# Performance work log

Hardware: AMD Instinct MI355X
Metric: run time of the kernel (lower is better)

The kernel has to match this reference:

```python
import jax, jax.numpy as jnp
import numpy as np

B, E, F, H, P = 1024, 300, 128, 512, 256


def _gru_cell(x, h, Wih, Whh, bih, bhh):
    # PyTorch GRUCell: gates ordered (r, z, n)
    gi = x @ Wih.T + bih
    gh = h @ Whh.T + bhh
    i_r, i_z, i_n = jnp.split(gi, 3, axis=-1)
    h_r, h_z, h_n = jnp.split(gh, 3, axis=-1)
    r = jax.nn.sigmoid(i_r + h_r)
    z = jax.nn.sigmoid(i_z + h_z)
    n = jnp.tanh(i_n + r * h_n)
    return (1.0 - z) * n + z * h


def setup_inputs() -> dict:
    key = jax.random.key(0)
    ks = jax.random.split(key, 24)
    rn = lambda k, s: (jax.random.normal(k, s, dtype=jnp.float32) * 0.05)
    inp = {
        'step_input': jax.random.normal(ks[0], (B, E), dtype=jnp.float32),
        'target_feat': jax.random.normal(ks[1], (B, F), dtype=jnp.float32),
        'obj_feats': jax.random.normal(ks[2], (B, P, F), dtype=jnp.float32),
        'hidden_1': jax.random.normal(ks[3], (B, H), dtype=jnp.float32),
        'hidden_2': jax.random.normal(ks[4], (B, H), dtype=jnp.float32),
        # Linear weights, shape (out, in), bias=False
        'W_td1': rn(ks[5], (128, H)),
        'W_td2': rn(ks[6], (128, F)),
        'W_td3': rn(ks[7], (128, E)),
        'W_td': rn(ks[8], (128, 128)),
        'W_feat': rn(ks[9], (H, F)),
        'W_hidd': rn(ks[10], (H, H)),
        'W_att': rn(ks[11], (1, H)),
        'W_l1': rn(ks[12], (128, F)),
        'W_l2': rn(ks[13], (128, H)),
        'W_l': rn(ks[14], (128, 128)),
        # GRUCell params (bias=True by default in torch)
        'gru1_Wih': rn(ks[15], (3 * H, 128)),
        'gru1_Whh': rn(ks[16], (3 * H, H)),
        'gru1_bih': rn(ks[17], (3 * H,)),
        'gru1_bhh': rn(ks[18], (3 * H,)),
        'gru2_Wih': rn(ks[19], (3 * H, 128)),
        'gru2_Whh': rn(ks[20], (3 * H, H)),
        'gru2_bih': rn(ks[21], (3 * H,)),
        'gru2_bhh': rn(ks[22], (3 * H,)),
    }
    return inp


def reference(step_input, target_feat, obj_feats, hidden_1, hidden_2,
              W_td1, W_td2, W_td3, W_td,
              W_feat, W_hidd, W_att, W_l1, W_l2, W_l,
              gru1_Wih, gru1_Whh, gru1_bih, gru1_bhh,
              gru2_Wih, gru2_Whh, gru2_bih, gru2_bhh):
    # Top-down input fusion
    td = step_input @ W_td3.T + hidden_2 @ W_td1.T + target_feat @ W_td2.T
    td = jax.nn.relu(jnp.tanh(td) @ W_td.T)
    h1 = _gru_cell(td, hidden_1, gru1_Wih, gru1_Whh, gru1_bih, gru1_bhh)

    # Soft attention over proposals
    combined = jnp.tanh(
        jnp.einsum('bpf,hf->bph', obj_feats, W_feat)
        + (h1 @ W_hidd.T)[:, None, :]
    )  # (B, P, H)
    scores = jnp.einsum('bph,oh->bpo', combined, W_att)  # (B, P, 1)
    masks = jax.nn.softmax(scores, axis=1)  # (B, P, 1)
    attended = jnp.sum(obj_feats * masks, axis=1)  # (B, F)

    # Language input fusion
    lang = jnp.tanh(attended @ W_l1.T + h1 @ W_l2.T)
    lang = jax.nn.relu(lang @ W_l.T)
    h2 = _gru_cell(lang, hidden_2, gru2_Wih, gru2_Whh, gru2_bih, gru2_bhh)
    return (h1, h2, masks)
```

## Files before the change

kernel.cpp:

```cpp
#include <hip/hip_runtime.h>
#include <hip/hip_bf16.h>
#include <stdint.h>


typedef __attribute__((ext_vector_type(8))) short short8;
typedef __attribute__((ext_vector_type(4))) float f32x4;

#define DEV static __device__ __forceinline__

DEV float rcp_f(float x) { return __builtin_amdgcn_rcpf(x); }
DEV float fast_tanh(float x) {
  float ax = fabsf(x);
  float e = __expf(2.0f * ax);
  float t = 1.0f - 2.0f * rcp_f(e + 1.0f);
  return x < 0.0f ? -t : t;
}
DEV float fast_sigmoid(float x) { return rcp_f(1.0f + __expf(-x)); }
DEV unsigned short f2bf(float x) {
  unsigned u = __float_as_uint(x);
  u += 0x7fffu + ((u >> 16) & 1u);
  return (unsigned short)(u >> 16);
}
DEV float bf2f(unsigned short s) { return __uint_as_float(((unsigned)s) << 16); }

#define NJOBS 17
struct CvtJobs {
  const float* src[NJOBS];
  unsigned short* dst[NJOBS];
};
__global__ __launch_bounds__(256) void cvt_all(CvtJobs jobs) {
  const int cum[NJOBS + 1] = {0, 327680, 458752, 983040, 1507328, 1548288,
                              1613824, 1630208, 1646592, 1712128, 1974272,
                              1990656, 2056192, 2072576, 2269184, 3055616,
                              3252224, 4038656};
  const int Ks[NJOBS]  = {300, 128, 512, 512, 300, 512, 128, 128, 128, 512,
                          128, 512, 128, 128, 512, 128, 512};
  const int Kps[NJOBS] = {320, 128, 512, 512, 320, 512, 128, 128, 128, 512,
                          128, 512, 128, 128, 512, 128, 512};
  int g = blockIdx.x * 256 + (int)threadIdx.x;
  if (g >= 4038656) return;
  int j = 0;
  while (g >= cum[j + 1]) ++j;
  const int local = g - cum[j];
  const int Kp = Kps[j], K = Ks[j];
  const int r = local / Kp, c = local - r * Kp;
  jobs.dst[j][local] = (c < K) ? f2bf(jobs.src[j][(size_t)r * K + c])
                               : (unsigned short)0;
}

#define FACC 1
#define FRELU (1 << 2)
#define FTANH (2 << 2)
__global__ __launch_bounds__(256) void gemm_bf16(
    const unsigned short* __restrict__ A, const unsigned short* __restrict__ W,
    const float* __restrict__ bias, float* __restrict__ C,
    unsigned short* __restrict__ Cb, int M, int N, int K,
    int lda, int ldw, int flags)
{
  __shared__ unsigned short As[64][40];
  __shared__ unsigned short Ws[64][40];
  const int bm = blockIdx.x * 64, bn = blockIdx.y * 64;
  const int tid = (int)threadIdx.x;
  const int w = tid >> 6, l = tid & 63, l15 = l & 15, lg = l >> 4;
  const int wr = w >> 1, wc = w & 1;
  const int srow = tid >> 2, sq = tid & 3;

  f32x4 acc[2][2] = {};

  for (int k0 = 0; k0 < K; k0 += 32) {
    const uint4 va = *(const uint4*)(A + (size_t)(bm + srow) * lda + k0 + sq * 8);
    const uint4 vw = *(const uint4*)(W + (size_t)(bn + srow) * ldw + k0 + sq * 8);
    __syncthreads();
    *(uint4*)&As[srow][sq * 8] = va;
    *(uint4*)&Ws[srow][sq * 8] = vw;
    __syncthreads();

    short8 af[2], bf[2];
#pragma unroll
    for (int mi = 0; mi < 2; ++mi) {
      const int ar = wr * 32 + mi * 16 + l15;
      union { short8 s8; uint2 u[2]; } f;
      f.u[0] = *(const uint2*)&As[ar][lg * 4];
      f.u[1] = *(const uint2*)&As[ar][16 + lg * 4];
      af[mi] = f.s8;
    }
#pragma unroll
    for (int ni = 0; ni < 2; ++ni) {
      const int br = wc * 32 + ni * 16 + l15;
      union { short8 s8; uint2 u[2]; } f;
      f.u[0] = *(const uint2*)&Ws[br][lg * 4];
      f.u[1] = *(const uint2*)&Ws[br][16 + lg * 4];
      bf[ni] = f.s8;
    }
#pragma unroll
    for (int mi = 0; mi < 2; ++mi)
#pragma unroll
      for (int ni = 0; ni < 2; ++ni)
        acc[mi][ni] = __builtin_amdgcn_mfma_f32_16x16x32_bf16(
            af[mi], bf[ni], acc[mi][ni], 0, 0, 0);
  }

  const int act = flags >> 2;
#pragma unroll
  for (int mi = 0; mi < 2; ++mi)
#pragma unroll
    for (int ni = 0; ni < 2; ++ni)
#pragma unroll
      for (int r = 0; r < 4; ++r) {
        const int m = bm + wr * 32 + mi * 16 + lg * 4 + r;
        const int n = bn + wc * 32 + ni * 16 + l15;
        float v = acc[mi][ni][r];
        if (bias) v += bias[n];
        if (flags & FACC) v += C[(size_t)m * N + n];
        if (act == 1) v = fmaxf(v, 0.0f);
        else if (act == 2) v = fast_tanh(v);
        if (C) C[(size_t)m * N + n] = v;
        if (Cb) Cb[(size_t)m * N + n] = f2bf(v);
      }
}

__global__ __launch_bounds__(256) void gru_combine(
    const unsigned short* __restrict__ gi, const unsigned short* __restrict__ gh,
    const float* __restrict__ hprev, float* __restrict__ hnew,
    unsigned short* __restrict__ hnewb)
{
  const int i4 = blockIdx.x * 256 + (int)threadIdx.x;
  const int b = i4 >> 7, j4 = (i4 & 127) * 4;
  const unsigned short* gib = gi + (size_t)b * 1536 + j4;
  const unsigned short* ghb = gh + (size_t)b * 1536 + j4;
  union { uint2 u; unsigned short s[4]; } gr, gz, gn, hr, hz, hn;
  gr.u = *(const uint2*)(gib);        hr.u = *(const uint2*)(ghb);
  gz.u = *(const uint2*)(gib + 512);  hz.u = *(const uint2*)(ghb + 512);
  gn.u = *(const uint2*)(gib + 1024); hn.u = *(const uint2*)(ghb + 1024);
  const float4 hp = *(const float4*)&hprev[(size_t)b * 512 + j4];
  const float hpv[4] = {hp.x, hp.y, hp.z, hp.w};
  float o[4];
  union { uint2 u; unsigned short s[4]; } ob;
#pragma unroll
  for (int k = 0; k < 4; ++k) {
    const float r = fast_sigmoid(bf2f(gr.s[k]) + bf2f(hr.s[k]));
    const float z = fast_sigmoid(bf2f(gz.s[k]) + bf2f(hz.s[k]));
    const float n = fast_tanh(bf2f(gn.s[k]) + r * bf2f(hn.s[k]));
    o[k] = (1.0f - z) * n + z * hpv[k];
    ob.s[k] = f2bf(o[k]);
  }
  float4 ov; ov.x = o[0]; ov.y = o[1]; ov.z = o[2]; ov.w = o[3];
  *(float4*)&hnew[(size_t)b * 512 + j4] = ov;
  if (hnewb) *(uint2*)&hnewb[(size_t)b * 512 + j4] = ob.u;
}

__global__ __launch_bounds__(256) void attn_kernel(
    const float* __restrict__ obj, const unsigned short* __restrict__ wf,
    const float* __restrict__ hb, const float* __restrict__ watt,
    float* __restrict__ masks_out, unsigned short* __restrict__ attb)
{
  __shared__ float scores[256];
  __shared__ float red[8];
  __shared__ float attw[4][128];
  __shared__ float hbs[512];
  __shared__ float wats[512];

  const int b = (int)blockIdx.x;
  const int tid = (int)threadIdx.x;
  const int w = tid >> 6, l = tid & 63;
  const int l15 = l & 15, lg = l >> 4;

  const float* objb = obj + (size_t)b * 32768;
  const float* hbb = hb + (size_t)b * 512;

  for (int i = tid; i < 512; i += 256) { hbs[i] = hbb[i]; wats[i] = watt[i]; }

  short8 afrag[4][4];
#pragma unroll
  for (int mt = 0; mt < 4; ++mt) {
    const int p = w * 64 + mt * 16 + l15;
#pragma unroll
    for (int kt = 0; kt < 4; ++kt) {
      union { short8 s8; unsigned u[4]; } fr;
#pragma unroll
      for (int half = 0; half < 2; ++half) {
        const int f = kt * 32 + half * 16 + lg * 4;
        const float4 v = *(const float4*)&objb[p * 128 + f];
        fr.u[half * 2 + 0] = (unsigned)f2bf(v.x) | ((unsigned)f2bf(v.y) << 16);
        fr.u[half * 2 + 1] = (unsigned)f2bf(v.z) | ((unsigned)f2bf(v.w) << 16);
      }
      afrag[mt][kt] = fr.s8;
    }
  }
  __syncthreads();

  float ps[4][4] = {};
  unsigned cur[4][4], nxt[4][4];
  {
    const unsigned short* wrow = wf + (size_t)l15 * 128;
#pragma unroll
    for (int kt = 0; kt < 4; ++kt) {
      const uint2 lo = *(const uint2*)&wrow[kt * 32 + lg * 4];
      const uint2 hi = *(const uint2*)&wrow[kt * 32 + 16 + lg * 4];
      cur[kt][0] = lo.x; cur[kt][1] = lo.y; cur[kt][2] = hi.x; cur[kt][3] = hi.y;
    }
  }
  for (int nc = 0; nc < 32; ++nc) {
    if (nc < 31) {
      const unsigned short* wrow = wf + (size_t)((nc + 1) * 16 + l15) * 128;
#pragma unroll
      for (int kt = 0; kt < 4; ++kt) {
        const uint2 lo = *(const uint2*)&wrow[kt * 32 + lg * 4];
        const uint2 hi = *(const uint2*)&wrow[kt * 32 + 16 + lg * 4];
        nxt[kt][0] = lo.x; nxt[kt][1] = lo.y; nxt[kt][2] = hi.x; nxt[kt][3] = hi.y;
      }
    }
    const int hh = nc * 16 + l15;
    const float hbv = hbs[hh];
    const float wav = wats[hh];
#pragma unroll
    for (int mt = 0; mt < 4; ++mt) {
      f32x4 acc = {0.f, 0.f, 0.f, 0.f};
#pragma unroll
      for (int kt = 0; kt < 4; ++kt) {
        union { short8 s8; unsigned u[4]; } f;
        f.u[0] = cur[kt][0]; f.u[1] = cur[kt][1];
        f.u[2] = cur[kt][2]; f.u[3] = cur[kt][3];
        acc = __builtin_amdgcn_mfma_f32_16x16x32_bf16(afrag[mt][kt], f.s8, acc, 0, 0, 0);
      }
#pragma unroll
      for (int r = 0; r < 4; ++r)
        ps[mt][r] += wav * fast_tanh(acc[r] + hbv);
    }
#pragma unroll
    for (int kt = 0; kt < 4; ++kt)
#pragma unroll
      for (int q = 0; q < 4; ++q) cur[kt][q] = nxt[kt][q];
  }

#pragma unroll
  for (int mt = 0; mt < 4; ++mt)
#pragma unroll
    for (int r = 0; r < 4; ++r) {
      float v = ps[mt][r];
      v += __shfl_xor(v, 1);
      v += __shfl_xor(v, 2);
      v += __shfl_xor(v, 4);
      v += __shfl_xor(v, 8);
      if (l15 == 0) scores[w * 64 + mt * 16 + lg * 4 + r] = v;
    }
  __syncthreads();

  const float s = scores[tid];
  float mx = s;
#pragma unroll
  for (int off = 32; off > 0; off >>= 1) mx = fmaxf(mx, __shfl_xor(mx, off));
  if (l == 0) red[w] = mx;
  __syncthreads();
  mx = fmaxf(fmaxf(red[0], red[1]), fmaxf(red[2], red[3]));
  const float e = __expf(s - mx);
  float sm = e;
#pragma unroll
  for (int off = 32; off > 0; off >>= 1) sm += __shfl_xor(sm, off);
  if (l == 0) red[4 + w] = sm;
  __syncthreads();
  const float mymask = e * rcp_f(red[4] + red[5] + red[6] + red[7]);
  masks_out[(size_t)b * 256 + tid] = mymask;

  float att_acc[8][4] = {};
#pragma unroll
  for (int mt = 0; mt < 4; ++mt) {
    const float mk = __shfl(mymask, mt * 16 + l15);
#pragma unroll
    for (int kt = 0; kt < 4; ++kt)
#pragma unroll
      for (int half = 0; half < 2; ++half)
#pragma unroll
        for (int j = 0; j < 4; ++j)
          att_acc[kt * 2 + half][j] += mk * bf2f((unsigned short)afrag[mt][kt][half * 4 + j]);
  }
#pragma unroll
  for (int slot = 0; slot < 8; ++slot)
#pragma unroll
    for (int j = 0; j < 4; ++j) {
      float v = att_acc[slot][j];
      v += __shfl_xor(v, 1);
      v += __shfl_xor(v, 2);
      v += __shfl_xor(v, 4);
      v += __shfl_xor(v, 8);
      if (l15 == 0) {
        const int kt = slot >> 1, half = slot & 1;
        attw[w][kt * 32 + half * 16 + lg * 4 + j] = v;
      }
    }
  __syncthreads();
  if (tid < 128)
    attb[(size_t)b * 128 + tid] =
        f2bf(attw[0][tid] + attw[1][tid] + attw[2][tid] + attw[3][tid]);
}

extern "C" void kernel_launch(void* const* d_in, const int* in_sizes, int n_in,
                              void* d_out, int out_size, void* d_ws, size_t ws_size,
                              hipStream_t stream) {
  (void)in_sizes; (void)n_in; (void)out_size; (void)ws_size;
  const float* step   = (const float*)d_in[0];
  const float* tf     = (const float*)d_in[1];
  const float* obj    = (const float*)d_in[2];
  const float* h1prev = (const float*)d_in[3];
  const float* h2prev = (const float*)d_in[4];
  const float* W_td1  = (const float*)d_in[5];
  const float* W_td2  = (const float*)d_in[6];
  const float* W_td3  = (const float*)d_in[7];
  const float* W_td   = (const float*)d_in[8];
  const float* W_feat = (const float*)d_in[9];
  const float* W_hidd = (const float*)d_in[10];
  const float* W_att  = (const float*)d_in[11];
  const float* W_l1   = (const float*)d_in[12];
  const float* W_l2   = (const float*)d_in[13];
  const float* W_l    = (const float*)d_in[14];
  const float* g1Wih  = (const float*)d_in[15];
  const float* g1Whh  = (const float*)d_in[16];
  const float* g1bih  = (const float*)d_in[17];
  const float* g1bhh  = (const float*)d_in[18];
  const float* g2Wih  = (const float*)d_in[19];
  const float* g2Whh  = (const float*)d_in[20];
  const float* g2bih  = (const float*)d_in[21];
  const float* g2bhh  = (const float*)d_in[22];

  float* h1    = (float*)d_out;
  float* h2    = (float*)d_out + 524288;
  float* masks = (float*)d_out + 1048576;

  unsigned short* wsb = (unsigned short*)d_ws;
  unsigned short* step_b  = wsb + 0;
  unsigned short* tf_b    = wsb + 327680;
  unsigned short* h1p_b   = wsb + 458752;
  unsigned short* h2p_b   = wsb + 983040;
  unsigned short* wtd3b   = wsb + 1507328;
  unsigned short* wtd1b   = wsb + 1548288;
  unsigned short* wtd2b   = wsb + 1613824;
  unsigned short* wtdb    = wsb + 1630208;
  unsigned short* wfeatb  = wsb + 1646592;
  unsigned short* whiddb  = wsb + 1712128;
  unsigned short* wl1b    = wsb + 1974272;
  unsigned short* wl2b    = wsb + 1990656;
  unsigned short* wlb     = wsb + 2056192;
  unsigned short* g1wihb  = wsb + 2072576;
  unsigned short* g1whhb  = wsb + 2269184;
  unsigned short* g2wihb  = wsb + 3055616;
  unsigned short* g2whhb  = wsb + 3252224;
  unsigned short* h1b     = wsb + 4038656;
  unsigned short* tdb     = wsb + 4562944;
  unsigned short* td2b    = wsb + 4694016;
  unsigned short* attb    = wsb + 4825088;
  unsigned short* langb   = wsb + 4956160;
  unsigned short* lang2b  = wsb + 5087232;
  unsigned short* gi_b    = wsb + 5218304;
  unsigned short* gh_b    = wsb + 6791168;
  float* scratchf = (float*)(wsb + 6791168);

  const dim3 blk(256);

  CvtJobs jobs;
  const float* srcs[NJOBS] = {step, tf, h1prev, h2prev, W_td3, W_td1, W_td2,
                              W_td, W_feat, W_hidd, W_l1, W_l2, W_l,
                              g1Wih, g1Whh, g2Wih, g2Whh};
  unsigned short* dsts[NJOBS] = {step_b, tf_b, h1p_b, h2p_b, wtd3b, wtd1b,
                                 wtd2b, wtdb, wfeatb, whiddb, wl1b, wl2b, wlb,
                                 g1wihb, g1whhb, g2wihb, g2whhb};
  for (int i = 0; i < NJOBS; ++i) { jobs.src[i] = srcs[i]; jobs.dst[i] = dsts[i]; }
  cvt_all<<<dim3(15776), blk, 0, stream>>>(jobs);

  gemm_bf16<<<dim3(16, 2), blk, 0, stream>>>(step_b, wtd3b, nullptr, scratchf, nullptr, 1024, 128, 320, 320, 320, 0);
  gemm_bf16<<<dim3(16, 2), blk, 0, stream>>>(h2p_b,  wtd1b, nullptr, scratchf, nullptr, 1024, 128, 512, 512, 512, FACC);
  gemm_bf16<<<dim3(16, 2), blk, 0, stream>>>(tf_b,   wtd2b, nullptr, scratchf, tdb,     1024, 128, 128, 128, 128, FACC | FTANH);
  gemm_bf16<<<dim3(16, 2), blk, 0, stream>>>(tdb,    wtdb,  nullptr, nullptr,  td2b,    1024, 128, 128, 128, 128, FRELU);

  gemm_bf16<<<dim3(16, 24), blk, 0, stream>>>(td2b,  g1wihb, g1bih, nullptr, gi_b, 1024, 1536, 128, 128, 128, 0);
  gemm_bf16<<<dim3(16, 24), blk, 0, stream>>>(h1p_b, g1whhb, g1bhh, nullptr, gh_b, 1024, 1536, 512, 512, 512, 0);
  gru_combine<<<dim3(512), blk, 0, stream>>>(gi_b, gh_b, h1prev, h1, h1b);

  gemm_bf16<<<dim3(16, 8), blk, 0, stream>>>(h1b, whiddb, nullptr, scratchf, nullptr, 1024, 512, 512, 512, 512, 0);

  attn_kernel<<<dim3(1024), blk, 0, stream>>>(obj, wfeatb, scratchf, W_att, masks, attb);

  gemm_bf16<<<dim3(16, 2), blk, 0, stream>>>(attb,  wl1b, nullptr, scratchf, nullptr, 1024, 128, 128, 128, 128, 0);
  gemm_bf16<<<dim3(16, 2), blk, 0, stream>>>(h1b,   wl2b, nullptr, scratchf, langb,   1024, 128, 512, 512, 512, FACC | FTANH);
  gemm_bf16<<<dim3(16, 2), blk, 0, stream>>>(langb, wlb,  nullptr, nullptr,  lang2b,  1024, 128, 128, 128, 128, FRELU);

  gemm_bf16<<<dim3(16, 24), blk, 0, stream>>>(lang2b, g2wihb, g2bih, nullptr, gi_b, 1024, 1536, 128, 128, 128, 0);
  gemm_bf16<<<dim3(16, 24), blk, 0, stream>>>(h2p_b,  g2whhb, g2bhh, nullptr, gh_b, 1024, 1536, 512, 512, 512, 0);
  gru_combine<<<dim3(512), blk, 0, stream>>>(gi_b, gh_b, h2prev, h2, nullptr);
}
```

Baseline: 496.7 us.

## Concatenate GEMM operands, vectorize conversion, and widen attention to 512 threads

Input and weight conversion now writes concatenated K-dimension buffers, so the three top-down GEMMs and the two language GEMMs each collapse into one GEMM. This removes three launches and the float accumulate round-trips. The conversion kernel processes four elements per thread through templated per-job block ranges instead of a per-element job search. The attention kernel moves to 512 threads with fewer rows per wave, loads W_feat directly instead of through a register double buffer, and computes the softmax in a single wave. The tanh and sigmoid helpers switch to exp2-based forms, and gru_combine writes h1 straight into the concatenated buffer.

```diff
diff --git a/kernel.cpp b/kernel.cpp
--- a/kernel.cpp
+++ b/kernel.cpp
@@ -9,43 +9,65 @@
 #define DEV static __device__ __forceinline__
 
 DEV float rcp_f(float x) { return __builtin_amdgcn_rcpf(x); }
-DEV float fast_tanh(float x) {
-  float ax = fabsf(x);
-  float e = __expf(2.0f * ax);
-  float t = 1.0f - 2.0f * rcp_f(e + 1.0f);
-  return x < 0.0f ? -t : t;
-}
-DEV float fast_sigmoid(float x) { return rcp_f(1.0f + __expf(-x)); }
+DEV float exp2_f(float x) { return __builtin_amdgcn_exp2f(x); }
+DEV float tanh2(float x) {
+  const float t = exp2_f(-2.885390082f * x);
+  return __builtin_fmaf(2.0f, rcp_f(1.0f + t), -1.0f);
+}
+DEV float sigm2(float x) { return rcp_f(1.0f + exp2_f(-1.442695041f * x)); }
+DEV float exp_f(float x) { return exp2_f(1.442695041f * x); }
 DEV unsigned short f2bf(float x) {
   unsigned u = __float_as_uint(x);
   u += 0x7fffu + ((u >> 16) & 1u);
   return (unsigned short)(u >> 16);
 }
 DEV float bf2f(unsigned short s) { return __uint_as_float(((unsigned)s) << 16); }
-
-#define NJOBS 17
-struct CvtJobs {
-  const float* src[NJOBS];
-  unsigned short* dst[NJOBS];
+DEV unsigned pk2(float a, float b) {
+  return (unsigned)f2bf(a) | ((unsigned)f2bf(b) << 16);
+}
+
+template<int K, int Kp, int LD, int C0>
+DEV void cvt_job(const float* __restrict__ src, unsigned short* __restrict__ dst,
+                 int q) {
+  constexpr int Q = Kp / 4;
+  const int r = q / Q;
+  const int c = (q - r * Q) * 4;
+  union { uint2 u; unsigned short s[4]; } o;
+  if (K == Kp || c < K) {
+    const float4 v = *(const float4*)&src[(size_t)r * K + c];
+    o.s[0] = f2bf(v.x); o.s[1] = f2bf(v.y); o.s[2] = f2bf(v.z); o.s[3] = f2bf(v.w);
+  } else {
+    o.u.x = 0u; o.u.y = 0u;
+  }
+  *(uint2*)&dst[(size_t)r * LD + C0 + c] = o.u;
+}
+
+struct CvtArgs {
+  const float *step, *tf, *h2p, *h1p, *wtd3, *wtd2, *wtd1, *wtd, *wfeat,
+              *whidd, *wl1, *wl2, *wl, *g1wih, *g1whh, *g2wih, *g2whh;
+  unsigned short *tdcatA, *h1pb, *tdcatW, *wtdb, *wfeatb, *whiddb,
+                 *langcatW, *wlb, *g1wihb, *g1whhb, *g2wihb, *g2whhb;
 };
-__global__ __launch_bounds__(256) void cvt_all(CvtJobs jobs) {
-  const int cum[NJOBS + 1] = {0, 327680, 458752, 983040, 1507328, 1548288,
-                              1613824, 1630208, 1646592, 1712128, 1974272,
-                              1990656, 2056192, 2072576, 2269184, 3055616,
-                              3252224, 4038656};
-  const int Ks[NJOBS]  = {300, 128, 512, 512, 300, 512, 128, 128, 128, 512,
-                          128, 512, 128, 128, 512, 128, 512};
-  const int Kps[NJOBS] = {320, 128, 512, 512, 320, 512, 128, 128, 128, 512,
-                          128, 512, 128, 128, 512, 128, 512};
-  int g = blockIdx.x * 256 + (int)threadIdx.x;
-  if (g >= 4038656) return;
-  int j = 0;
-  while (g >= cum[j + 1]) ++j;
-  const int local = g - cum[j];
-  const int Kp = Kps[j], K = Ks[j];
-  const int r = local / Kp, c = local - r * Kp;
-  jobs.dst[j][local] = (c < K) ? f2bf(jobs.src[j][(size_t)r * K + c])
-                               : (unsigned short)0;
+
+__global__ __launch_bounds__(256) void cvt_all(CvtArgs a) {
+  const int bid = (int)blockIdx.x, tid = (int)threadIdx.x;
+  if      (bid <  320) cvt_job<300, 320, 960,   0>(a.step,  a.tdcatA,   bid         * 256 + tid);
+  else if (bid <  448) cvt_job<128, 128, 960, 320>(a.tf,    a.tdcatA,   (bid -  320) * 256 + tid);
+  else if (bid <  960) cvt_job<512, 512, 960, 448>(a.h2p,   a.tdcatA,   (bid -  448) * 256 + tid);
+  else if (bid < 1472) cvt_job<512, 512, 512,   0>(a.h1p,   a.h1pb,     (bid -  960) * 256 + tid);
+  else if (bid < 1512) cvt_job<300, 320, 960,   0>(a.wtd3,  a.tdcatW,   (bid - 1472) * 256 + tid);
+  else if (bid < 1528) cvt_job<128, 128, 960, 320>(a.wtd2,  a.tdcatW,   (bid - 1512) * 256 + tid);
+  else if (bid < 1592) cvt_job<512, 512, 960, 448>(a.wtd1,  a.tdcatW,   (bid - 1528) * 256 + tid);
+  else if (bid < 1608) cvt_job<128, 128, 128,   0>(a.wtd,   a.wtdb,     (bid - 1592) * 256 + tid);
+  else if (bid < 1672) cvt_job<128, 128, 128,   0>(a.wfeat, a.wfeatb,   (bid - 1608) * 256 + tid);
+  else if (bid < 1928) cvt_job<512, 512, 512,   0>(a.whidd, a.whiddb,   (bid - 1672) * 256 + tid);
+  else if (bid < 1944) cvt_job<128, 128, 640,   0>(a.wl1,   a.langcatW, (bid - 1928) * 256 + tid);
+  else if (bid < 2008) cvt_job<512, 512, 640, 128>(a.wl2,   a.langcatW, (bid - 1944) * 256 + tid);
+  else if (bid < 2024) cvt_job<128, 128, 128,   0>(a.wl,    a.wlb,      (bid - 2008) * 256 + tid);
+  else if (bid < 2216) cvt_job<128, 128, 128,   0>(a.g1wih, a.g1wihb,   (bid - 2024) * 256 + tid);
+  else if (bid < 2984) cvt_job<512, 512, 512,   0>(a.g1whh, a.g1whhb,   (bid - 2216) * 256 + tid);
+  else if (bid < 3176) cvt_job<128, 128, 128,   0>(a.g2wih, a.g2wihb,   (bid - 2984) * 256 + tid);
+  else if (bid < 3944) cvt_job<512, 512, 512,   0>(a.g2whh, a.g2whhb,   (bid - 3176) * 256 + tid);
 }
 
 #define FACC 1
@@ -113,7 +135,7 @@
         if (bias) v += bias[n];
         if (flags & FACC) v += C[(size_t)m * N + n];
         if (act == 1) v = fmaxf(v, 0.0f);
-        else if (act == 2) v = fast_tanh(v);
+        else if (act == 2) v = tanh2(v);
         if (C) C[(size_t)m * N + n] = v;
         if (Cb) Cb[(size_t)m * N + n] = f2bf(v);
       }
@@ -122,7 +144,7 @@
 __global__ __launch_bounds__(256) void gru_combine(
     const unsigned short* __restrict__ gi, const unsigned short* __restrict__ gh,
     const float* __restrict__ hprev, float* __restrict__ hnew,
-    unsigned short* __restrict__ hnewb)
+    unsigned short* __restrict__ hnewb, int ldhb)
 {
   const int i4 = blockIdx.x * 256 + (int)threadIdx.x;
   const int b = i4 >> 7, j4 = (i4 & 127) * 4;
@@ -138,25 +160,25 @@
   union { uint2 u; unsigned short s[4]; } ob;
 #pragma unroll
   for (int k = 0; k < 4; ++k) {
-    const float r = fast_sigmoid(bf2f(gr.s[k]) + bf2f(hr.s[k]));
-    const float z = fast_sigmoid(bf2f(gz.s[k]) + bf2f(hz.s[k]));
-    const float n = fast_tanh(bf2f(gn.s[k]) + r * bf2f(hn.s[k]));
+    const float r = sigm2(bf2f(gr.s[k]) + bf2f(hr.s[k]));
+    const float z = sigm2(bf2f(gz.s[k]) + bf2f(hz.s[k]));
+    const float n = tanh2(bf2f(gn.s[k]) + r * bf2f(hn.s[k]));
     o[k] = (1.0f - z) * n + z * hpv[k];
     ob.s[k] = f2bf(o[k]);
   }
   float4 ov; ov.x = o[0]; ov.y = o[1]; ov.z = o[2]; ov.w = o[3];
   *(float4*)&hnew[(size_t)b * 512 + j4] = ov;
-  if (hnewb) *(uint2*)&hnewb[(size_t)b * 512 + j4] = ob.u;
-}
-
-__global__ __launch_bounds__(256) void attn_kernel(
+  if (hnewb) *(uint2*)&hnewb[(size_t)b * ldhb + j4] = ob.u;
+}
+
+__global__ __launch_bounds__(512, 6) void attn_kernel(
     const float* __restrict__ obj, const unsigned short* __restrict__ wf,
     const float* __restrict__ hb, const float* __restrict__ watt,
     float* __restrict__ masks_out, unsigned short* __restrict__ attb)
 {
-  __shared__ float scores[256];
-  __shared__ float red[8];
-  __shared__ float attw[4][128];
+  __shared__ __align__(16) float scores[256];
+  __shared__ __align__(16) float smasks[256];
+  __shared__ float attw[8][128];
   __shared__ float hbs[512];
   __shared__ float wats[512];
 
@@ -167,74 +189,63 @@
 
   const float* objb = obj + (size_t)b * 32768;
   const float* hbb = hb + (size_t)b * 512;
-
-  for (int i = tid; i < 512; i += 256) { hbs[i] = hbb[i]; wats[i] = watt[i]; }
-
-  short8 afrag[4][4];
-#pragma unroll
-  for (int mt = 0; mt < 4; ++mt) {
-    const int p = w * 64 + mt * 16 + l15;
+  hbs[tid] = hbb[tid];
+  wats[tid] = watt[tid];
+
+  short8 afrag[2][4];
+#pragma unroll
+  for (int mt = 0; mt < 2; ++mt) {
+    const float* prow = objb + (size_t)(w * 32 + mt * 16 + l15) * 128;
 #pragma unroll
     for (int kt = 0; kt < 4; ++kt) {
       union { short8 s8; unsigned u[4]; } fr;
 #pragma unroll
       for (int half = 0; half < 2; ++half) {
-        const int f = kt * 32 + half * 16 + lg * 4;
-        const float4 v = *(const float4*)&objb[p * 128 + f];
-        fr.u[half * 2 + 0] = (unsigned)f2bf(v.x) | ((unsigned)f2bf(v.y) << 16);
-        fr.u[half * 2 + 1] = (unsigned)f2bf(v.z) | ((unsigned)f2bf(v.w) << 16);
+        const float4 v = *(const float4*)&prow[kt * 32 + half * 16 + lg * 4];
+        fr.u[half * 2 + 0] = pk2(v.x, v.y);
+        fr.u[half * 2 + 1] = pk2(v.z, v.w);
       }
       afrag[mt][kt] = fr.s8;
     }
   }
   __syncthreads();
 
-  float ps[4][4] = {};
-  unsigned cur[4][4], nxt[4][4];
-  {
-    const unsigned short* wrow = wf + (size_t)l15 * 128;
-#pragma unroll
-    for (int kt = 0; kt < 4; ++kt) {
-      const uint2 lo = *(const uint2*)&wrow[kt * 32 + lg * 4];
-      const uint2 hi = *(const uint2*)&wrow[kt * 32 + 16 + lg * 4];
-      cur[kt][0] = lo.x; cur[kt][1] = lo.y; cur[kt][2] = hi.x; cur[kt][3] = hi.y;
-    }
-  }
+  float ps[2][4] = {};
   for (int nc = 0; nc < 32; ++nc) {
-    if (nc < 31) {
-      const unsigned short* wrow = wf + (size_t)((nc + 1) * 16 + l15) * 128;
-#pragma unroll
-      for (int kt = 0; kt < 4; ++kt) {
-        const uint2 lo = *(const uint2*)&wrow[kt * 32 + lg * 4];
-        const uint2 hi = *(const uint2*)&wrow[kt * 32 + 16 + lg * 4];
-        nxt[kt][0] = lo.x; nxt[kt][1] = lo.y; nxt[kt][2] = hi.x; nxt[kt][3] = hi.y;
-      }
-    }
     const int hh = nc * 16 + l15;
+    const unsigned short* wrow = wf + (size_t)hh * 128;
+    f32x4 a0 = {0.f, 0.f, 0.f, 0.f}, a1 = {0.f, 0.f, 0.f, 0.f};
+#pragma unroll
+    for (int kk = 0; kk < 2; ++kk) {
+      short8 b0, b1;
+      {
+        union { short8 s8; uint2 u[2]; } f;
+        f.u[0] = *(const uint2*)&wrow[(kk * 2) * 32 + lg * 4];
+        f.u[1] = *(const uint2*)&wrow[(kk * 2) * 32 + 16 + lg * 4];
+        b0 = f.s8;
+      }
+      {
+        union { short8 s8; uint2 u[2]; } f;
+        f.u[0] = *(const uint2*)&wrow[(kk * 2 + 1) * 32 + lg * 4];
+        f.u[1] = *(const uint2*)&wrow[(kk * 2 + 1) * 32 + 16 + lg * 4];
+        b1 = f.s8;
+      }
+      a0 = __builtin_amdgcn_mfma_f32_16x16x32_bf16(afrag[0][kk * 2],     b0, a0, 0, 0, 0);
+      a0 = __builtin_amdgcn_mfma_f32_16x16x32_bf16(afrag[0][kk * 2 + 1], b1, a0, 0, 0, 0);
+      a1 = __builtin_amdgcn_mfma_f32_16x16x32_bf16(afrag[1][kk * 2],     b0, a1, 0, 0, 0);
+      a1 = __builtin_amdgcn_mfma_f32_16x16x32_bf16(afrag[1][kk * 2 + 1], b1, a1, 0, 0, 0);
+    }
     const float hbv = hbs[hh];
     const float wav = wats[hh];
 #pragma unroll
-    for (int mt = 0; mt < 4; ++mt) {
-      f32x4 acc = {0.f, 0.f, 0.f, 0.f};
-#pragma unroll
-      for (int kt = 0; kt < 4; ++kt) {
-        union { short8 s8; unsigned u[4]; } f;
-        f.u[0] = cur[kt][0]; f.u[1] = cur[kt][1];
-        f.u[2] = cur[kt][2]; f.u[3] = cur[kt][3];
-        acc = __builtin_amdgcn_mfma_f32_16x16x32_bf16(afrag[mt][kt], f.s8, acc, 0, 0, 0);
-      }
-#pragma unroll
-      for (int r = 0; r < 4; ++r)
-        ps[mt][r] += wav * fast_tanh(acc[r] + hbv);
-    }
-#pragma unroll
-    for (int kt = 0; kt < 4; ++kt)
-#pragma unroll
-      for (int q = 0; q < 4; ++q) cur[kt][q] = nxt[kt][q];
-  }
-
-#pragma unroll
-  for (int mt = 0; mt < 4; ++mt)
+    for (int r = 0; r < 4; ++r) {
+      ps[0][r] = __builtin_fmaf(wav, tanh2(a0[r] + hbv), ps[0][r]);
+      ps[1][r] = __builtin_fmaf(wav, tanh2(a1[r] + hbv), ps[1][r]);
+    }
+  }
+
+#pragma unroll
+  for (int mt = 0; mt < 2; ++mt)
 #pragma unroll
     for (int r = 0; r < 4; ++r) {
       float v = ps[mt][r];
@@ -242,37 +253,40 @@
       v += __shfl_xor(v, 2);
       v += __shfl_xor(v, 4);
       v += __shfl_xor(v, 8);
-      if (l15 == 0) scores[w * 64 + mt * 16 + lg * 4 + r] = v;
+      if (l15 == 0) scores[w * 32 + mt * 16 + lg * 4 + r] = v;
     }
   __syncthreads();
 
-  const float s = scores[tid];
-  float mx = s;
-#pragma unroll
-  for (int off = 32; off > 0; off >>= 1) mx = fmaxf(mx, __shfl_xor(mx, off));
-  if (l == 0) red[w] = mx;
+  if (w == 0) {
+    const float4 sv = *(const float4*)&scores[l * 4];
+    float mx = fmaxf(fmaxf(sv.x, sv.y), fmaxf(sv.z, sv.w));
+#pragma unroll
+    for (int off = 32; off > 0; off >>= 1) mx = fmaxf(mx, __shfl_xor(mx, off));
+    const float e0 = exp_f(sv.x - mx), e1 = exp_f(sv.y - mx);
+    const float e2 = exp_f(sv.z - mx), e3 = exp_f(sv.w - mx);
+    float sm = (e0 + e1) + (e2 + e3);
+#pragma unroll
+    for (int off = 32; off > 0; off >>= 1) sm += __shfl_xor(sm, off);
+    const float rt = rcp_f(sm);
+    float4 mk; mk.x = e0 * rt; mk.y = e1 * rt; mk.z = e2 * rt; mk.w = e3 * rt;
+    *(float4*)&masks_out[(size_t)b * 256 + l * 4] = mk;
+    *(float4*)&smasks[l * 4] = mk;
+  }
   __syncthreads();
-  mx = fmaxf(fmaxf(red[0], red[1]), fmaxf(red[2], red[3]));
-  const float e = __expf(s - mx);
-  float sm = e;
-#pragma unroll
-  for (int off = 32; off > 0; off >>= 1) sm += __shfl_xor(sm, off);
-  if (l == 0) red[4 + w] = sm;
-  __syncthreads();
-  const float mymask = e * rcp_f(red[4] + red[5] + red[6] + red[7]);
-  masks_out[(size_t)b * 256 + tid] = mymask;
 
   float att_acc[8][4] = {};
 #pragma unroll
-  for (int mt = 0; mt < 4; ++mt) {
-    const float mk = __shfl(mymask, mt * 16 + l15);
+  for (int mt = 0; mt < 2; ++mt) {
+    const float mk = smasks[w * 32 + mt * 16 + l15];
 #pragma unroll
     for (int kt = 0; kt < 4; ++kt)
 #pragma unroll
       for (int half = 0; half < 2; ++half)
 #pragma unroll
         for (int j = 0; j < 4; ++j)
-          att_acc[kt * 2 + half][j] += mk * bf2f((unsigned short)afrag[mt][kt][half * 4 + j]);
+          att_acc[kt * 2 + half][j] =
+              __builtin_fmaf(mk, bf2f((unsigned short)afrag[mt][kt][half * 4 + j]),
+                             att_acc[kt * 2 + half][j]);
   }
 #pragma unroll
   for (int slot = 0; slot < 8; ++slot)
@@ -289,9 +303,12 @@
       }
     }
   __syncthreads();
-  if (tid < 128)
-    attb[(size_t)b * 128 + tid] =
-        f2bf(attw[0][tid] + attw[1][tid] + attw[2][tid] + attw[3][tid]);
+  if (tid < 128) {
+    float s = 0.f;
+#pragma unroll
+    for (int q = 0; q < 8; ++q) s += attw[q][tid];
+    attb[(size_t)b * 640 + tid] = f2bf(s);
+  }
 }
 
 extern "C" void kernel_launch(void* const* d_in, const int* in_sizes, int n_in,
@@ -327,63 +344,54 @@
   float* masks = (float*)d_out + 1048576;
 
   unsigned short* wsb = (unsigned short*)d_ws;
-  unsigned short* step_b  = wsb + 0;
-  unsigned short* tf_b    = wsb + 327680;
-  unsigned short* h1p_b   = wsb + 458752;
-  unsigned short* h2p_b   = wsb + 983040;
-  unsigned short* wtd3b   = wsb + 1507328;
-  unsigned short* wtd1b   = wsb + 1548288;
-  unsigned short* wtd2b   = wsb + 1613824;
-  unsigned short* wtdb    = wsb + 1630208;
-  unsigned short* wfeatb  = wsb + 1646592;
-  unsigned short* whiddb  = wsb + 1712128;
-  unsigned short* wl1b    = wsb + 1974272;
-  unsigned short* wl2b    = wsb + 1990656;
-  unsigned short* wlb     = wsb + 2056192;
-  unsigned short* g1wihb  = wsb + 2072576;
-  unsigned short* g1whhb  = wsb + 2269184;
-  unsigned short* g2wihb  = wsb + 3055616;
-  unsigned short* g2whhb  = wsb + 3252224;
-  unsigned short* h1b     = wsb + 4038656;
-  unsigned short* tdb     = wsb + 4562944;
-  unsigned short* td2b    = wsb + 4694016;
-  unsigned short* attb    = wsb + 4825088;
-  unsigned short* langb   = wsb + 4956160;
-  unsigned short* lang2b  = wsb + 5087232;
-  unsigned short* gi_b    = wsb + 5218304;
-  unsigned short* gh_b    = wsb + 6791168;
+  unsigned short* tdcatA   = wsb + 0;
+  unsigned short* h1p_b    = wsb + 983040;
+  unsigned short* tdcatW   = wsb + 1507328;
+  unsigned short* wtdb     = wsb + 1630208;
+  unsigned short* wfeatb   = wsb + 1646592;
+  unsigned short* whiddb   = wsb + 1712128;
+  unsigned short* langcatW = wsb + 1974272;
+  unsigned short* wlb      = wsb + 2056192;
+  unsigned short* g1wihb   = wsb + 2072576;
+  unsigned short* g1whhb   = wsb + 2269184;
+  unsigned short* g2wihb   = wsb + 3055616;
+  unsigned short* g2whhb   = wsb + 3252224;
+  unsigned short* tdb      = wsb + 4038656;
+  unsigned short* td2b     = wsb + 4169728;
+  unsigned short* langcatA = wsb + 4300800;
+  unsigned short* langb    = wsb + 4956160;
+  unsigned short* lang2b   = wsb + 5087232;
+  unsigned short* gi_b     = wsb + 5218304;
+  unsigned short* gh_b     = wsb + 6791168;
   float* scratchf = (float*)(wsb + 6791168);
 
   const dim3 blk(256);
 
-  CvtJobs jobs;
-  const float* srcs[NJOBS] = {step, tf, h1prev, h2prev, W_td3, W_td1, W_td2,
-                              W_td, W_feat, W_hidd, W_l1, W_l2, W_l,
-                              g1Wih, g1Whh, g2Wih, g2Whh};
-  unsigned short* dsts[NJOBS] = {step_b, tf_b, h1p_b, h2p_b, wtd3b, wtd1b,
-                                 wtd2b, wtdb, wfeatb, whiddb, wl1b, wl2b, wlb,
-                                 g1wihb, g1whhb, g2wihb, g2whhb};
-  for (int i = 0; i < NJOBS; ++i) { jobs.src[i] = srcs[i]; jobs.dst[i] = dsts[i]; }
-  cvt_all<<<dim3(15776), blk, 0, stream>>>(jobs);
-
-  gemm_bf16<<<dim3(16, 2), blk, 0, stream>>>(step_b, wtd3b, nullptr, scratchf, nullptr, 1024, 128, 320, 320, 320, 0);
-  gemm_bf16<<<dim3(16, 2), blk, 0, stream>>>(h2p_b,  wtd1b, nullptr, scratchf, nullptr, 1024, 128, 512, 512, 512, FACC);
-  gemm_bf16<<<dim3(16, 2), blk, 0, stream>>>(tf_b,   wtd2b, nullptr, scratchf, tdb,     1024, 128, 128, 128, 128, FACC | FTANH);
-  gemm_bf16<<<dim3(16, 2), blk, 0, stream>>>(tdb,    wtdb,  nullptr, nullptr,  td2b,    1024, 128, 128, 128, 128, FRELU);
+  CvtArgs a;
+  a.step = step; a.tf = tf; a.h2p = h2prev; a.h1p = h1prev;
+  a.wtd3 = W_td3; a.wtd2 = W_td2; a.wtd1 = W_td1; a.wtd = W_td;
+  a.wfeat = W_feat; a.whidd = W_hidd; a.wl1 = W_l1; a.wl2 = W_l2; a.wl = W_l;
+  a.g1wih = g1Wih; a.g1whh = g1Whh; a.g2wih = g2Wih; a.g2whh = g2Whh;
+  a.tdcatA = tdcatA; a.h1pb = h1p_b; a.tdcatW = tdcatW; a.wtdb = wtdb;
+  a.wfeatb = wfeatb; a.whiddb = whiddb; a.langcatW = langcatW; a.wlb = wlb;
+  a.g1wihb = g1wihb; a.g1whhb = g1whhb; a.g2wihb = g2wihb; a.g2whhb = g2whhb;
+  cvt_all<<<dim3(3944), blk, 0, stream>>>(a);
+
+  gemm_bf16<<<dim3(16, 2), blk, 0, stream>>>(tdcatA, tdcatW, nullptr, nullptr, tdb,  1024, 128, 960, 960, 960, FTANH);
+  gemm_bf16<<<dim3(16, 2), blk, 0, stream>>>(tdb,    wtdb,   nullptr, nullptr, td2b, 1024, 128, 128, 128, 128, FRELU);
 
   gemm_bf16<<<dim3(16, 24), blk, 0, stream>>>(td2b,  g1wihb, g1bih, nullptr, gi_b, 1024, 1536, 128, 128, 128, 0);
   gemm_bf16<<<dim3(16, 24), blk, 0, stream>>>(h1p_b, g1whhb, g1bhh, nullptr, gh_b, 1024, 1536, 512, 512, 512, 0);
-  gru_combine<<<dim3(512), blk, 0, stream>>>(gi_b, gh_b, h1prev, h1, h1b);
-
-  gemm_bf16<<<dim3(16, 8), blk, 0, stream>>>(h1b, whiddb, nullptr, scratchf, nullptr, 1024, 512, 512, 512, 512, 0);
-
-  attn_kernel<<<dim3(1024), blk, 0, stream>>>(obj, wfeatb, scratchf, W_att, masks, attb);
-
-  gemm_bf16<<<dim3(16, 2), blk, 0, stream>>>(attb,  wl1b, nullptr, scratchf, nullptr, 1024, 128, 128, 128, 128, 0);
-  gemm_bf16<<<dim3(16, 2), blk, 0, stream>>>(h1b,   wl2b, nullptr, scratchf, langb,   1024, 128, 512, 512, 512, FACC | FTANH);
-  gemm_bf16<<<dim3(16, 2), blk, 0, stream>>>(langb, wlb,  nullptr, nullptr,  lang2b,  1024, 128, 128, 128, 128, FRELU);
-
-  gemm_bf16<<<dim3(16, 24), blk, 0, stream>>>(lang2b, g2wihb, g2bih, nullptr, gi_b, 1024, 1536, 128, 128, 128, 0);
-  gemm_bf16<<<dim3(16, 24), blk, 0, stream>>>(h2p_b,  g2whhb, g2bhh, nullptr, gh_b, 1024, 1536, 512, 512, 512, 0);
-  gru_combine<<<dim3(512), blk, 0, stream>>>(gi_b, gh_b, h2prev, h2, nullptr);
-}
+  gru_combine<<<dim3(512), blk, 0, stream>>>(gi_b, gh_b, h1prev, h1, langcatA + 128, 640);
+
+  gemm_bf16<<<dim3(16, 8), blk, 0, stream>>>(langcatA + 128, whiddb, nullptr, scratchf, nullptr, 1024, 512, 512, 640, 512, 0);
+
+  attn_kernel<<<dim3(1024), dim3(512), 0, stream>>>(obj, wfeatb, scratchf, W_att, masks, langcatA);
+
+  gemm_bf16<<<dim3(16, 2), blk, 0, stream>>>(langcatA, langcatW, nullptr, nullptr, langb,  1024, 128, 640, 640, 640, FTANH);
+  gemm_bf16<<<dim3(16, 2), blk, 0, stream>>>(langb,    wlb,      nullptr, nullptr, lang2b, 1024, 128, 128, 128, 128, FRELU);
+
+  gemm_bf16<<<dim3(16, 24), blk, 0, stream>>>(lang2b,       g2wihb, g2bih, nullptr, gi_b, 1024, 1536, 128, 128, 128, 0);
+  gemm_bf16<<<dim3(16, 24), blk, 0, stream>>>(tdcatA + 448, g2whhb, g2bhh, nullptr, gh_b, 1024, 1536, 512, 960, 512, 0);
+  gru_combine<<<dim3(512), blk, 0, stream>>>(gi_b, gh_b, h2prev, h2, nullptr, 0);
+}
```

Result: slower. 562.2 us (+13.2%).
